# Kernel tuning notes

Measured on AMD Instinct MI355X. Metric: run time of the kernel, lower is better.

## Reference

```python
import jax, jax.numpy as jnp
import numpy as np

V_DIM, L_DIM, EMBED, HEADS = 256, 768, 2048, 8
HEAD_DIM = EMBED // HEADS
SCALING = HEAD_DIM ** -0.5
NEG = -10000.0


def _linear_params(key, fan_in, fan_out, kaiming=True):
    kw, _ = jax.random.split(key)
    std = (2.0 / fan_out) ** 0.5 if kaiming else fan_in ** -0.5
    W = jax.random.normal(kw, (fan_in, fan_out), dtype=jnp.float32) * std
    b = jnp.zeros((fan_out,), dtype=jnp.float32)
    return W, b


def setup_inputs() -> dict:
    key = jax.random.key(0)
    ks = jax.random.split(key, 10)
    B, Hv, Hl = 8, 4096, 256
    v = jax.random.normal(ks[0], (B, Hv, V_DIM), dtype=jnp.float32)
    l = jax.random.normal(ks[1], (B, Hl, L_DIM), dtype=jnp.float32)
    attention_mask_v = jax.random.randint(ks[2], (B, Hv), 0, 2, dtype=jnp.int32)
    attention_mask_l = jax.random.randint(ks[3], (B, Hl), 0, 2, dtype=jnp.int32)
    Wq_v, bq_v = _linear_params(ks[4], V_DIM, EMBED)
    Wk_l, bk_l = _linear_params(ks[5], L_DIM, EMBED)
    Wval_v, bval_v = _linear_params(ks[6], V_DIM, EMBED)
    Wval_l, bval_l = _linear_params(ks[7], L_DIM, EMBED)
    Wo_v, bo_v = _linear_params(ks[8], EMBED, V_DIM, kaiming=False)
    Wo_l, bo_l = _linear_params(ks[9], EMBED, L_DIM, kaiming=False)
    return {"v": v, "l": l,
            "attention_mask_v": attention_mask_v, "attention_mask_l": attention_mask_l,
            "Wq_v": Wq_v, "bq_v": bq_v, "Wk_l": Wk_l, "bk_l": bk_l,
            "Wval_v": Wval_v, "bval_v": bval_v, "Wval_l": Wval_l, "bval_l": bval_l,
            "Wo_v": Wo_v, "bo_v": bo_v, "Wo_l": Wo_l, "bo_l": bo_l}


def _split_heads(x, B, S):  # [B,S,E] -> [B,H,S,D]
    return x.reshape(B, S, HEADS, HEAD_DIM).transpose(0, 2, 1, 3)


def reference(v, l, attention_mask_v, attention_mask_l,
              Wq_v, bq_v, Wk_l, bk_l, Wval_v, bval_v, Wval_l, bval_l,
              Wo_v, bo_v, Wo_l, bo_l):
    B, Hv, _ = v.shape
    _, Hl, _ = l.shape
    q = _split_heads((v @ Wq_v + bq_v) * SCALING, B, Hv)      # [B,H,Hv,D]
    k = _split_heads(l @ Wk_l + bk_l, B, Hl)                  # [B,H,Hl,D]
    v_value = _split_heads(v @ Wval_v + bval_v, B, Hv)        # [B,H,Hv,D]
    l_value = _split_heads(l @ Wval_l + bval_l, B, Hl)        # [B,H,Hl,D]

    attn = jnp.einsum('bhqd,bhkd->bhqk', q, k)                # [B,H,Hv,Hl]
    attn = jnp.where(attention_mask_l[:, None, None, :] != 0, attn, NEG)
    attn = jnp.where(attention_mask_v[:, None, :, None] != 0, attn, NEG)

    attn_v = jax.nn.softmax(attn, axis=-1)                    # softmax over Hl
    attn_l = jax.nn.softmax(attn.transpose(0, 1, 3, 2), axis=-1)  # over Hv

    out_v = jnp.einsum('bhqk,bhkd->bhqd', attn_v, l_value)    # [B,H,Hv,D]
    out_l = jnp.einsum('bhkq,bhqd->bhkd', attn_l, v_value)    # [B,H,Hl,D]
    out_v = out_v.transpose(0, 2, 1, 3).reshape(B, Hv, EMBED)
    out_l = out_l.transpose(0, 2, 1, 3).reshape(B, Hl, EMBED)
    return (out_v @ Wo_v + bo_v, out_l @ Wo_l + bo_l)
```

## Files before the change

kernel.cpp:

```cpp
#include <hip/hip_runtime.h>
#include <cstdint>

using u16 = unsigned short;
using u32 = unsigned int;

typedef short s16x8 __attribute__((ext_vector_type(8)));
typedef float f32x4 __attribute__((ext_vector_type(4)));

__device__ __forceinline__ u16 f2bf(float f) {
  u32 u = __float_as_uint(f);
  return (u16)((u + 0x7fffu + ((u >> 16) & 1u)) >> 16);
}
__device__ __forceinline__ float bf2f(u16 u) {
  return __uint_as_float(((u32)u) << 16);
}

__device__ __forceinline__ void gld16(const void* g, void* l) {
  __builtin_amdgcn_global_load_lds(
      (const __attribute__((address_space(1))) u32*)g,
      (__attribute__((address_space(3))) u32*)l, 16, 0, 0);
}

#define MFMA(a, b, c) __builtin_amdgcn_mfma_f32_16x16x32_bf16((a), (b), (c), 0, 0, 0)

template<int OUT_MODE, bool HAS_BIAS>
__global__ __launch_bounds__(256, 2)
void gemm_nt(const u16* __restrict__ A, const u16* __restrict__ B,
             const float* __restrict__ bias, void* __restrict__ C,
             int M, int N, int K, int ldOut)
{
  __shared__ __align__(16) u16 smem[17408];
  u16* As = smem;
  u16* Bs = smem + 4096;
  const int tid = threadIdx.x, wv = tid >> 6, ln = tid & 63;
  const int wm = wv >> 1, wn = wv & 1;
  const long m0 = (long)blockIdx.y * 128, n0 = (long)blockIdx.x * 128;

  f32x4 acc[4][4] = {};
  for (int k0 = 0; k0 < K; k0 += 32) {
    #pragma unroll
    for (int j = 0; j < 2; j++) {
      const int ub = j*256 + wv*64, u = ub + ln;
      gld16(A + (m0 + (u >> 2)) * K + k0 + (u & 3) * 8, As + ub * 8);
    }
    #pragma unroll
    for (int j = 0; j < 2; j++) {
      const int ub = j*256 + wv*64, u = ub + ln;
      gld16(B + (n0 + (u >> 2)) * K + k0 + (u & 3) * 8, Bs + ub * 8);
    }
    __syncthreads();
    {
      s16x8 af[4], bf[4];
      const int kk = (ln >> 4) * 8;
      #pragma unroll
      for (int i = 0; i < 4; i++) af[i] = *(const s16x8*)&As[(wm*64 + i*16 + (ln & 15)) * 32 + kk];
      #pragma unroll
      for (int i = 0; i < 4; i++) bf[i] = *(const s16x8*)&Bs[(wn*64 + i*16 + (ln & 15)) * 32 + kk];
      #pragma unroll
      for (int i = 0; i < 4; i++)
        #pragma unroll
        for (int j = 0; j < 4; j++)
          acc[i][j] = MFMA(af[i], bf[j], acc[i][j]);
    }
    __syncthreads();
  }

  if constexpr (OUT_MODE == 2) {
    u16* ct = smem;
    #pragma unroll
    for (int i = 0; i < 4; i++)
      #pragma unroll
      for (int j = 0; j < 4; j++)
        #pragma unroll
        for (int jj = 0; jj < 4; jj++) {
          const int cl = wn*64 + j*16 + (ln & 15);
          const int rl = wm*64 + i*16 + (ln >> 4) * 4 + jj;
          float v = acc[i][j][jj];
          if constexpr (HAS_BIAS) v += bias[n0 + cl];
          ct[cl * 136 + rl] = f2bf(v);
        }
    __syncthreads();
    const long S = ldOut;
    const long bb = m0 / S;
    u16* T = (u16*)C + bb * (long)(N - 1) * S;
    #pragma unroll
    for (int t = 0; t < 8; t++) {
      const int u = t*256 + tid;
      const int cl = u >> 4, r8 = (u & 15) * 8;
      *(s16x8*)&T[(n0 + cl) * S + (m0 + r8)] = *(const s16x8*)&ct[cl * 136 + r8];
    }
  } else {
    #pragma unroll
    for (int i = 0; i < 4; i++)
      #pragma unroll
      for (int jj = 0; jj < 4; jj++) {
        const long r = m0 + wm*64 + i*16 + (ln >> 4) * 4 + jj;
        #pragma unroll
        for (int j = 0; j < 4; j++) {
          const long col = n0 + wn*64 + j*16 + (ln & 15);
          float v = acc[i][j][jj];
          if constexpr (HAS_BIAS) v += bias[col];
          if constexpr (OUT_MODE == 0) ((float*)C)[r * ldOut + col] = v;
          else                         ((u16*)C)[r * ldOut + col] = f2bf(v);
        }
      }
  }
}

__global__ __launch_bounds__(256, 2)
void attn_v(u16* __restrict__ Q, const u16* __restrict__ Kw,
            const u16* __restrict__ VlT, const int* __restrict__ mask_v,
            const int* __restrict__ mask_l, const int* __restrict__ anylp,
            int b_base)
{
  __shared__ __align__(16) u16 As[64*72];
  __shared__ __align__(16) u16 Bs[256*72];
  __shared__ __align__(16) u16 Ps[64*264];
  __shared__ float red[256];

  const int qt = blockIdx.x;
  const int bl = blockIdx.y >> 3, h = blockIdx.y & 7;
  const int b = b_base + bl;
  const int tid = threadIdx.x, wv = tid >> 6, ln = tid & 63;

  u16* Qb = Q + (long)(bl*4096 + qt*64) * 2048 + h*256;
  const u16* Kb = Kw + (long)(b*256) * 2048 + h*256;
  const u16* Vb = VlT + (long)(b*8 + h) * 65536;

  const int al = anylp[b];
  float mlf[4], rf[4][4];
  #pragma unroll
  for (int j = 0; j < 4; j++)
    mlf[j] = mask_l[b*256 + wv*64 + j*16 + (ln & 15)] ? 1.f : 0.f;
  #pragma unroll
  for (int i = 0; i < 4; i++)
    #pragma unroll
    for (int jj = 0; jj < 4; jj++)
      rf[i][jj] = (al && mask_v[b*4096 + qt*64 + i*16 + (ln >> 4)*4 + jj]) ? 1.f : 0.f;

  f32x4 acc[4][4] = {};
  for (int d0 = 0; d0 < 256; d0 += 64) {
    #pragma unroll
    for (int j = 0; j < 2; j++) {
      const int u = j*256 + tid, r = u >> 3, c = (u & 7) * 8;
      *(s16x8*)&As[r*72 + c] = *(const s16x8*)(Qb + (long)r*2048 + d0 + c);
    }
    #pragma unroll
    for (int j = 0; j < 8; j++) {
      const int u = j*256 + tid, r = u >> 3, c = (u & 7) * 8;
      *(s16x8*)&Bs[r*72 + c] = *(const s16x8*)(Kb + (long)r*2048 + d0 + c);
    }
    __syncthreads();
    #pragma unroll
    for (int ks = 0; ks < 2; ks++) {
      s16x8 af[4], bf[4];
      const int kk = ks*32 + (ln >> 4) * 8;
      #pragma unroll
      for (int i = 0; i < 4; i++) af[i] = *(const s16x8*)&As[(i*16 + (ln & 15))*72 + kk];
      #pragma unroll
      for (int j = 0; j < 4; j++) bf[j] = *(const s16x8*)&Bs[(wv*64 + j*16 + (ln & 15))*72 + kk];
      #pragma unroll
      for (int i = 0; i < 4; i++)
        #pragma unroll
        for (int j = 0; j < 4; j++)
          acc[i][j] = MFMA(af[i], bf[j], acc[i][j]);
    }
    __syncthreads();
  }

  #pragma unroll
  for (int i = 0; i < 4; i++)
    #pragma unroll
    for (int j = 0; j < 4; j++)
      #pragma unroll
      for (int jj = 0; jj < 4; jj++) {
        const float s = acc[i][j][jj];
        acc[i][j][jj] = (rf[i][jj] != 0.f) ? mlf[j] * __expf(s) : 1.0f;
      }
  #pragma unroll
  for (int i = 0; i < 4; i++)
    #pragma unroll
    for (int jj = 0; jj < 4; jj++) {
      float t = acc[i][0][jj] + acc[i][1][jj] + acc[i][2][jj] + acc[i][3][jj];
      t += __shfl_xor(t, 1); t += __shfl_xor(t, 2);
      t += __shfl_xor(t, 4); t += __shfl_xor(t, 8);
      if ((ln & 15) == 0) red[wv*64 + i*16 + (ln >> 4)*4 + jj] = t;
    }
  __syncthreads();
  float inv[4][4];
  #pragma unroll
  for (int i = 0; i < 4; i++)
    #pragma unroll
    for (int jj = 0; jj < 4; jj++) {
      const int r = i*16 + (ln >> 4)*4 + jj;
      inv[i][jj] = 1.0f / (red[r] + red[64 + r] + red[128 + r] + red[192 + r]);
    }
  #pragma unroll
  for (int i = 0; i < 4; i++)
    #pragma unroll
    for (int j = 0; j < 4; j++)
      #pragma unroll
      for (int jj = 0; jj < 4; jj++)
        Ps[(i*16 + (ln >> 4)*4 + jj)*264 + wv*64 + j*16 + (ln & 15)] =
            f2bf(acc[i][j][jj] * inv[i][jj]);
  __syncthreads();

  f32x4 acc2[4][4] = {};
  for (int c0 = 0; c0 < 256; c0 += 64) {
    #pragma unroll
    for (int j = 0; j < 8; j++) {
      const int u = j*256 + tid, r = u >> 3, c = (u & 7) * 8;
      *(s16x8*)&Bs[r*72 + c] = *(const s16x8*)(Vb + (long)r*256 + c0 + c);
    }
    __syncthreads();
    #pragma unroll
    for (int ks = 0; ks < 2; ks++) {
      s16x8 af[4], bf[4];
      const int kk = ks*32 + (ln >> 4) * 8;
      #pragma unroll
      for (int i = 0; i < 4; i++) af[i] = *(const s16x8*)&Ps[(i*16 + (ln & 15))*264 + c0 + kk];
      #pragma unroll
      for (int j = 0; j < 4; j++) bf[j] = *(const s16x8*)&Bs[(wv*64 + j*16 + (ln & 15))*72 + kk];
      #pragma unroll
      for (int i = 0; i < 4; i++)
        #pragma unroll
        for (int j = 0; j < 4; j++)
          acc2[i][j] = MFMA(af[i], bf[j], acc2[i][j]);
    }
    __syncthreads();
  }
  #pragma unroll
  for (int i = 0; i < 4; i++)
    #pragma unroll
    for (int j = 0; j < 4; j++)
      #pragma unroll
      for (int jj = 0; jj < 4; jj++)
        Qb[(long)(i*16 + (ln >> 4)*4 + jj)*2048 + wv*64 + j*16 + (ln & 15)] =
            f2bf(acc2[i][j][jj]);
}

#define NSPLIT 8
__global__ __launch_bounds__(256, 2)
void attn_l_part(const u16* __restrict__ Q, const u16* __restrict__ Kw,
                 const u16* __restrict__ VvT, const int* __restrict__ mask_v,
                 const int* __restrict__ mask_l, const int* __restrict__ anyvp,
                 u16* __restrict__ Pp, float* __restrict__ Rp, int b_base)
{
  __shared__ __align__(16) u16 Ks[64*264];
  __shared__ __align__(16) u16 Vs[256*72];
  __shared__ __align__(16) u16 Es[64*72];
  __shared__ float red[256];
  __shared__ float mvf_s[64];
  u16* Qs = Vs;

  const int sp = blockIdx.x, kt = blockIdx.y;
  const int bl = blockIdx.z >> 3, h = blockIdx.z & 7;
  const int b = b_base + bl;
  const int tid = threadIdx.x, wv = tid >> 6, ln = tid & 63;

  const u16* Qb  = Q + (long)(bl*4096) * 2048 + h*256;
  const u16* Kb  = Kw + (long)(b*256 + kt*64) * 2048 + h*256;
  const u16* Vvb = VvT + (long)(bl*8 + h) * (256L*4096);

  #pragma unroll
  for (int j = 0; j < 8; j++) {
    const int u = j*256 + tid, r = u >> 5, c = (u & 31) * 8;
    *(s16x8*)&Ks[r*264 + c] = *(const s16x8*)(Kb + (long)r*2048 + c);
  }
  const int av = anyvp[b];
  float crf[4][4];
  #pragma unroll
  for (int i = 0; i < 4; i++)
    #pragma unroll
    for (int jj = 0; jj < 4; jj++)
      crf[i][jj] = (av && mask_l[b*256 + kt*64 + i*16 + (ln >> 4)*4 + jj]) ? 1.f : 0.f;

  float rsum[4][4] = {};
  f32x4 pacc[4][4] = {};

  const int qlo = sp * (4096 / NSPLIT), qhi = qlo + 4096 / NSPLIT;
  #pragma unroll 1
  for (int qc = qlo; qc < qhi; qc += 64) {
    if (tid < 64) mvf_s[tid] = mask_v[b*4096 + qc + tid] ? 1.f : 0.f;
    f32x4 sacc[4] = {};
    #pragma unroll 1
    for (int d0 = 0; d0 < 256; d0 += 64) {
      #pragma unroll
      for (int j = 0; j < 2; j++) {
        const int u = j*256 + tid, r = u >> 3, c = (u & 7) * 8;
        *(s16x8*)&Qs[r*72 + c] = *(const s16x8*)(Qb + (long)(qc + r)*2048 + d0 + c);
      }
      __syncthreads();
      #pragma unroll
      for (int ks = 0; ks < 2; ks++) {
        s16x8 af[4], bq;
        const int kk = ks*32 + (ln >> 4) * 8;
        #pragma unroll
        for (int i = 0; i < 4; i++) af[i] = *(const s16x8*)&Ks[(i*16 + (ln & 15))*264 + d0 + kk];
        bq = *(const s16x8*)&Qs[(wv*16 + (ln & 15))*72 + kk];
        #pragma unroll
        for (int i = 0; i < 4; i++) sacc[i] = MFMA(af[i], bq, sacc[i]);
      }
      __syncthreads();
    }
    const float mvf = mvf_s[wv*16 + (ln & 15)];
    #pragma unroll
    for (int i = 0; i < 4; i++)
      #pragma unroll
      for (int jj = 0; jj < 4; jj++) {
        const float x = (crf[i][jj] != 0.f) ? mvf * __expf(sacc[i][jj]) : 1.0f;
        float t = x;
        t += __shfl_xor(t, 1); t += __shfl_xor(t, 2);
        t += __shfl_xor(t, 4); t += __shfl_xor(t, 8);
        rsum[i][jj] += t;
        Es[(i*16 + (ln >> 4)*4 + jj)*72 + wv*16 + (ln & 15)] = f2bf(x);
      }
    __syncthreads();
    #pragma unroll
    for (int j = 0; j < 8; j++) {
      const int u = j*256 + tid, r = u >> 3, c = (u & 7) * 8;
      *(s16x8*)&Vs[r*72 + c] = *(const s16x8*)(Vvb + (long)r*4096 + qc + c);
    }
    __syncthreads();
    #pragma unroll
    for (int ks = 0; ks < 2; ks++) {
      s16x8 ae[4], bv[4];
      const int kk = ks*32 + (ln >> 4) * 8;
      #pragma unroll
      for (int i = 0; i < 4; i++) ae[i] = *(const s16x8*)&Es[(i*16 + (ln & 15))*72 + kk];
      #pragma unroll
      for (int j = 0; j < 4; j++) bv[j] = *(const s16x8*)&Vs[(wv*64 + j*16 + (ln & 15))*72 + kk];
      #pragma unroll
      for (int i = 0; i < 4; i++)
        #pragma unroll
        for (int j = 0; j < 4; j++)
          pacc[i][j] = MFMA(ae[i], bv[j], pacc[i][j]);
    }
    __syncthreads();
  }

  const long unit = ((long)blockIdx.z * 4 + kt) * NSPLIT + sp;
  u16*   Pb = Pp + unit * 16384;
  float* Rb = Rp + unit * 64;
  #pragma unroll
  for (int i = 0; i < 4; i++)
    #pragma unroll
    for (int jj = 0; jj < 4; jj++)
      if ((ln & 15) == 0) red[wv*64 + i*16 + (ln >> 4)*4 + jj] = rsum[i][jj];
  __syncthreads();
  if (tid < 64) Rb[tid] = red[tid] + red[64 + tid] + red[128 + tid] + red[192 + tid];
  #pragma unroll
  for (int i = 0; i < 4; i++)
    #pragma unroll
    for (int jj = 0; jj < 4; jj++) {
      const int r = i*16 + (ln >> 4)*4 + jj;
      #pragma unroll
      for (int j = 0; j < 4; j++)
        Pb[r*256 + wv*64 + j*16 + (ln & 15)] = f2bf(pacc[i][j][jj]);
    }
}

__global__ __launch_bounds__(256, 4)
void attn_l_red(const u16* __restrict__ Pp, const float* __restrict__ Rp,
                u16* __restrict__ ol, int b_base)
{
  __shared__ float rt[64];
  const int kt = blockIdx.x;
  const int bl = blockIdx.y >> 3, h = blockIdx.y & 7;
  const int b = b_base + bl;
  const int tid = threadIdx.x;
  const long ub = ((long)blockIdx.y * 4 + kt) * NSPLIT;

  if (tid < 64) {
    float t = 0.f;
    #pragma unroll
    for (int s = 0; s < NSPLIT; s++) t += Rp[(ub + s) * 64 + tid];
    rt[tid] = 1.0f / t;
  }
  __syncthreads();

  u16* olb = ol + (long)(b*256 + kt*64) * 2048 + h*256;
  #pragma unroll
  for (int it = 0; it < 8; it++) {
    const int idx = it*256 + tid;
    const int r = idx >> 5, c8 = (idx & 31) * 8;
    float a[8] = {};
    #pragma unroll
    for (int s = 0; s < NSPLIT; s++) {
      const s16x8 p = *(const s16x8*)&Pp[(ub + s)*16384 + r*256 + c8];
      #pragma unroll
      for (int e = 0; e < 8; e++) a[e] += bf2f((u16)p[e]);
    }
    const float sc = rt[r];
    s16x8 o;
    #pragma unroll
    for (int e = 0; e < 8; e++) o[e] = (short)f2bf(a[e] * sc);
    *(s16x8*)&olb[(long)r*2048 + c8] = o;
  }
}

__global__ void cvt_bf16_k(const float* __restrict__ x, u16* __restrict__ y, long n4) {
  const long i = (long)blockIdx.x * 256 + threadIdx.x;
  if (i < n4) {
    const float4 v = ((const float4*)x)[i];
    u32 lo = (u32)f2bf(v.x) | ((u32)f2bf(v.y) << 16);
    u32 hi = (u32)f2bf(v.z) | ((u32)f2bf(v.w) << 16);
    ((uint2*)y)[i] = make_uint2(lo, hi);
  }
}

__global__ void transpose_w(const float* __restrict__ W, u16* __restrict__ WT,
                            int K, int N, float scale) {
  __shared__ float t[64][65];
  const int k0 = blockIdx.y * 64, n0 = blockIdx.x * 64;
  const int tid = threadIdx.x;
  #pragma unroll
  for (int i = 0; i < 16; i++) {
    const int u = i*256 + tid, r = u >> 6, c = u & 63;
    t[r][c] = W[(long)(k0 + r) * N + n0 + c];
  }
  __syncthreads();
  #pragma unroll
  for (int i = 0; i < 16; i++) {
    const int u = i*256 + tid, r = u >> 6, c = u & 63;
    WT[(long)(n0 + r) * K + k0 + c] = f2bf(t[c][r] * scale);
  }
}

__global__ void scale_bias_k(const float* __restrict__ x, float* __restrict__ y,
                             int n, float s) {
  const int i = blockIdx.x * 256 + threadIdx.x;
  if (i < n) y[i] = x[i] * s;
}

__global__ void any_mask_k(const int* __restrict__ mv, const int* __restrict__ ml,
                           int* __restrict__ anyv, int* __restrict__ anyl) {
  __shared__ int s[256];
  const int b = blockIdx.x, t = threadIdx.x;
  int a = 0;
  for (int i = t; i < 4096; i += 256) a |= mv[b*4096 + i];
  s[t] = a; __syncthreads();
  for (int o = 128; o > 0; o >>= 1) { if (t < o) s[t] |= s[t + o]; __syncthreads(); }
  if (t == 0) anyv[b] = s[0] ? 1 : 0;
  __syncthreads();
  s[t] = ml[b*256 + t]; __syncthreads();
  for (int o = 128; o > 0; o >>= 1) { if (t < o) s[t] |= s[t + o]; __syncthreads(); }
  if (t == 0) anyl[b] = s[0] ? 1 : 0;
}

extern "C" void kernel_launch(void* const* d_in, const int* in_sizes, int n_in,
                              void* d_out, int out_size, void* d_ws, size_t ws_size,
                              hipStream_t stream)
{
  (void)in_sizes; (void)n_in; (void)out_size; (void)ws_size;
  const float* v   = (const float*)d_in[0];
  const float* l   = (const float*)d_in[1];
  const int*   mv  = (const int*)d_in[2];
  const int*   ml  = (const int*)d_in[3];
  const float* Wq  = (const float*)d_in[4];
  const float* bq  = (const float*)d_in[5];
  const float* Wk  = (const float*)d_in[6];
  const float* bk  = (const float*)d_in[7];
  const float* Wvv = (const float*)d_in[8];
  const float* bvv = (const float*)d_in[9];
  const float* Wvl = (const float*)d_in[10];
  const float* bvl = (const float*)d_in[11];
  const float* Wov = (const float*)d_in[12];
  const float* bov = (const float*)d_in[13];
  const float* Wol = (const float*)d_in[14];
  const float* bol = (const float*)d_in[15];

  char* w = (char*)d_ws;
  auto alloc = [&](size_t bytes) { char* p = w; w += (bytes + 255) & ~(size_t)255; return p; };
  u16*   l_bf = (u16*)alloc(1572864ull * 2);
  u16*   WqT  = (u16*)alloc(2048ull*256*2);
  u16*   WkT  = (u16*)alloc(2048ull*768*2);
  u16*   WvvT = (u16*)alloc(2048ull*256*2);
  u16*   WvlT = (u16*)alloc(2048ull*768*2);
  u16*   WovT = (u16*)alloc(256ull*2048*2);
  u16*   WolT = (u16*)alloc(768ull*2048*2);
  float* bq_s = (float*)alloc(2048*4);
  int*   anyv = (int*)alloc(256);
  int*   anyl = (int*)alloc(256);
  u16*   Kw   = (u16*)alloc(4194304ull * 2);
  u16*   VlT  = (u16*)alloc(4194304ull * 2);
  u16*   ol   = (u16*)alloc(4194304ull * 2);
  u16*   v_bf = (u16*)alloc(4194304ull * 2);
  u16*   Qw   = (u16*)alloc(33554432ull * 2);
  u16*   VvT  = (u16*)alloc(33554432ull * 2);
  u16*   Pp   = (u16*)alloc((size_t)32*4*NSPLIT*16384*2);
  float* Rp   = (float*)alloc((size_t)32*4*NSPLIT*64*4);

  const float SCL = 0.0625f;

  cvt_bf16_k<<<1536, 256, 0, stream>>>(l, l_bf, 393216);
  transpose_w<<<dim3(32, 4),  256, 0, stream>>>(Wq,  WqT,  256, 2048, SCL);
  transpose_w<<<dim3(32, 12), 256, 0, stream>>>(Wk,  WkT,  768, 2048, 1.0f);
  transpose_w<<<dim3(32, 4),  256, 0, stream>>>(Wvv, WvvT, 256, 2048, 1.0f);
  transpose_w<<<dim3(32, 12), 256, 0, stream>>>(Wvl, WvlT, 768, 2048, 1.0f);
  transpose_w<<<dim3(4, 32),  256, 0, stream>>>(Wov, WovT, 2048, 256, 1.0f);
  transpose_w<<<dim3(12, 32), 256, 0, stream>>>(Wol, WolT, 2048, 768, 1.0f);
  scale_bias_k<<<8, 256, 0, stream>>>(bq, bq_s, 2048, SCL);
  any_mask_k<<<8, 256, 0, stream>>>(mv, ml, anyv, anyl);

  gemm_nt<1, true><<<dim3(16, 16), 256, 0, stream>>>(l_bf, WkT,  bk,  Kw,  2048, 2048, 768, 2048);
  gemm_nt<2, true><<<dim3(16, 16), 256, 0, stream>>>(l_bf, WvlT, bvl, VlT, 2048, 2048, 768, 256);

  for (int g = 0; g < 2; g++) {
    const int b0 = 4 * g;
    cvt_bf16_k<<<4096, 256, 0, stream>>>(v + (long)g * 4194304, v_bf, 1048576);
    gemm_nt<1, true><<<dim3(16, 128), 256, 0, stream>>>(v_bf, WqT,  bq_s, Qw,  16384, 2048, 256, 2048);
    gemm_nt<2, true><<<dim3(16, 128), 256, 0, stream>>>(v_bf, WvvT, bvv,  VvT, 16384, 2048, 256, 4096);
    attn_l_part<<<dim3(NSPLIT, 4, 32), 256, 0, stream>>>(Qw, Kw, VvT, mv, ml, anyv, Pp, Rp, b0);
    attn_l_red<<<dim3(4, 32), 256, 0, stream>>>(Pp, Rp, ol, b0);
    attn_v<<<dim3(64, 32), 256, 0, stream>>>(Qw, Kw, VlT, mv, ml, anyl, b0);
    gemm_nt<0, true><<<dim3(2, 128), 256, 0, stream>>>(Qw, WovT, bov,
        (float*)d_out + (long)g * 4194304, 16384, 256, 2048, 256);
  }

  gemm_nt<0, true><<<dim3(6, 16), 256, 0, stream>>>(ol, WolT, bol,
      (float*)d_out + 8388608, 2048, 768, 2048, 768);
}
```

Before: 824.1 us.

## Load Q and V fragments directly into registers in attn_l_part, dropping LDS staging

The attn_l_part kernel no longer stages Q and transposed V tiles through shared memory. Each lane now loads its MFMA operand fragments straight from global memory into registers, and the mask is packed into a bitmask. This removes several __syncthreads per chunk and roughly halves LDS use, which lets the launch bound go from 2 to 3 blocks per CU. The cost is uncoalesced 16-byte global loads per lane and higher register pressure from holding the qf and vf fragments.

```diff
diff --git a/kernel.cpp b/kernel.cpp
--- a/kernel.cpp
+++ b/kernel.cpp
@@ -240,23 +240,21 @@
 }
 
 #define NSPLIT 8
-__global__ __launch_bounds__(256, 2)
+__global__ __launch_bounds__(256, 3)
 void attn_l_part(const u16* __restrict__ Q, const u16* __restrict__ Kw,
                  const u16* __restrict__ VvT, const int* __restrict__ mask_v,
                  const int* __restrict__ mask_l, const int* __restrict__ anyvp,
                  u16* __restrict__ Pp, float* __restrict__ Rp, int b_base)
 {
   __shared__ __align__(16) u16 Ks[64*264];
-  __shared__ __align__(16) u16 Vs[256*72];
   __shared__ __align__(16) u16 Es[64*72];
   __shared__ float red[256];
-  __shared__ float mvf_s[64];
-  u16* Qs = Vs;
 
   const int sp = blockIdx.x, kt = blockIdx.y;
   const int bl = blockIdx.z >> 3, h = blockIdx.z & 7;
   const int b = b_base + bl;
   const int tid = threadIdx.x, wv = tid >> 6, ln = tid & 63;
+  const int l = ln & 15, g = ln >> 4;
 
   const u16* Qb  = Q + (long)(bl*4096) * 2048 + h*256;
   const u16* Kb  = Kw + (long)(b*256 + kt*64) * 2048 + h*256;
@@ -268,73 +266,71 @@
     *(s16x8*)&Ks[r*264 + c] = *(const s16x8*)(Kb + (long)r*2048 + c);
   }
   const int av = anyvp[b];
-  float crf[4][4];
+  u32 cmask = 0;
   #pragma unroll
   for (int i = 0; i < 4; i++)
     #pragma unroll
     for (int jj = 0; jj < 4; jj++)
-      crf[i][jj] = (av && mask_l[b*256 + kt*64 + i*16 + (ln >> 4)*4 + jj]) ? 1.f : 0.f;
+      if (av && mask_l[b*256 + kt*64 + i*16 + g*4 + jj]) cmask |= 1u << (i*4 + jj);
 
   float rsum[4][4] = {};
   f32x4 pacc[4][4] = {};
+  __syncthreads();
 
   const int qlo = sp * (4096 / NSPLIT), qhi = qlo + 4096 / NSPLIT;
   #pragma unroll 1
   for (int qc = qlo; qc < qhi; qc += 64) {
-    if (tid < 64) mvf_s[tid] = mask_v[b*4096 + qc + tid] ? 1.f : 0.f;
+    const float mvf = mask_v[b*4096 + qc + wv*16 + l] ? 1.f : 0.f;
+
+    s16x8 qf[4][2];
+    #pragma unroll
+    for (int d0 = 0; d0 < 4; d0++)
+      #pragma unroll
+      for (int ks = 0; ks < 2; ks++)
+        qf[d0][ks] = *(const s16x8*)(Qb + (long)(qc + wv*16 + l)*2048 + d0*64 + ks*32 + g*8);
+
     f32x4 sacc[4] = {};
-    #pragma unroll 1
-    for (int d0 = 0; d0 < 256; d0 += 64) {
-      #pragma unroll
-      for (int j = 0; j < 2; j++) {
-        const int u = j*256 + tid, r = u >> 3, c = (u & 7) * 8;
-        *(s16x8*)&Qs[r*72 + c] = *(const s16x8*)(Qb + (long)(qc + r)*2048 + d0 + c);
+    #pragma unroll
+    for (int d0 = 0; d0 < 4; d0++)
+      #pragma unroll
+      for (int ks = 0; ks < 2; ks++) {
+        const int kk = d0*64 + ks*32 + g*8;
+        #pragma unroll
+        for (int i = 0; i < 4; i++)
+          sacc[i] = MFMA(*(const s16x8*)&Ks[(i*16 + l)*264 + kk], qf[d0][ks], sacc[i]);
       }
-      __syncthreads();
-      #pragma unroll
-      for (int ks = 0; ks < 2; ks++) {
-        s16x8 af[4], bq;
-        const int kk = ks*32 + (ln >> 4) * 8;
-        #pragma unroll
-        for (int i = 0; i < 4; i++) af[i] = *(const s16x8*)&Ks[(i*16 + (ln & 15))*264 + d0 + kk];
-        bq = *(const s16x8*)&Qs[(wv*16 + (ln & 15))*72 + kk];
-        #pragma unroll
-        for (int i = 0; i < 4; i++) sacc[i] = MFMA(af[i], bq, sacc[i]);
-      }
-      __syncthreads();
-    }
-    const float mvf = mvf_s[wv*16 + (ln & 15)];
+
+    s16x8 vf[4][2];
+    #pragma unroll
+    for (int j = 0; j < 4; j++)
+      #pragma unroll
+      for (int ks = 0; ks < 2; ks++)
+        vf[j][ks] = *(const s16x8*)(Vvb + (long)(wv*64 + j*16 + l)*4096 + qc + ks*32 + g*8);
+
     #pragma unroll
     for (int i = 0; i < 4; i++)
       #pragma unroll
       for (int jj = 0; jj < 4; jj++) {
-        const float x = (crf[i][jj] != 0.f) ? mvf * __expf(sacc[i][jj]) : 1.0f;
+        const float x = ((cmask >> (i*4 + jj)) & 1) ? mvf * __expf(sacc[i][jj]) : 1.0f;
         float t = x;
         t += __shfl_xor(t, 1); t += __shfl_xor(t, 2);
         t += __shfl_xor(t, 4); t += __shfl_xor(t, 8);
         rsum[i][jj] += t;
-        Es[(i*16 + (ln >> 4)*4 + jj)*72 + wv*16 + (ln & 15)] = f2bf(x);
+        Es[(i*16 + g*4 + jj)*72 + wv*16 + l] = f2bf(x);
       }
     __syncthreads();
-    #pragma unroll
-    for (int j = 0; j < 8; j++) {
-      const int u = j*256 + tid, r = u >> 3, c = (u & 7) * 8;
-      *(s16x8*)&Vs[r*72 + c] = *(const s16x8*)(Vvb + (long)r*4096 + qc + c);
-    }
-    __syncthreads();
+
     #pragma unroll
     for (int ks = 0; ks < 2; ks++) {
-      s16x8 ae[4], bv[4];
-      const int kk = ks*32 + (ln >> 4) * 8;
-      #pragma unroll
-      for (int i = 0; i < 4; i++) ae[i] = *(const s16x8*)&Es[(i*16 + (ln & 15))*72 + kk];
-      #pragma unroll
-      for (int j = 0; j < 4; j++) bv[j] = *(const s16x8*)&Vs[(wv*64 + j*16 + (ln & 15))*72 + kk];
+      s16x8 ae[4];
+      const int kk = ks*32 + g*8;
+      #pragma unroll
+      for (int i = 0; i < 4; i++) ae[i] = *(const s16x8*)&Es[(i*16 + l)*72 + kk];
       #pragma unroll
       for (int i = 0; i < 4; i++)
         #pragma unroll
         for (int j = 0; j < 4; j++)
-          pacc[i][j] = MFMA(ae[i], bv[j], pacc[i][j]);
+          pacc[i][j] = MFMA(ae[i], vf[j][ks], pacc[i][j]);
     }
     __syncthreads();
   }
@@ -346,17 +342,17 @@
   for (int i = 0; i < 4; i++)
     #pragma unroll
     for (int jj = 0; jj < 4; jj++)
-      if ((ln & 15) == 0) red[wv*64 + i*16 + (ln >> 4)*4 + jj] = rsum[i][jj];
+      if (l == 0) red[wv*64 + i*16 + g*4 + jj] = rsum[i][jj];
   __syncthreads();
   if (tid < 64) Rb[tid] = red[tid] + red[64 + tid] + red[128 + tid] + red[192 + tid];
   #pragma unroll
   for (int i = 0; i < 4; i++)
     #pragma unroll
     for (int jj = 0; jj < 4; jj++) {
-      const int r = i*16 + (ln >> 4)*4 + jj;
+      const int r = i*16 + g*4 + jj;
       #pragma unroll
       for (int j = 0; j < 4; j++)
-        Pb[r*256 + wv*64 + j*16 + (ln & 15)] = f2bf(pacc[i][j][jj]);
+        Pb[r*256 + wv*64 + j*16 + l] = f2bf(pacc[i][j][jj]);
     }
 }
 
```

Measured after the change: 808.3 us. About the same (-1.9%).
